# Kernel optimization log

Measured on AMD Instinct MI355X. Metric: run time of the kernel, lower is better.

The kernel has to match this reference:

```python
import jax, jax.numpy as jnp
import numpy as np
import math

BS, SEQ, EMB, BD = 4, 2048, 512, 8
H = EMB // BD


def setup_inputs() -> dict:
    key = jax.random.key(0)
    ks = jax.random.split(key, 7)
    s = lambda fan: 1.0 / np.sqrt(fan)
    x = jax.random.normal(ks[0], (BS, SEQ, EMB), jnp.float32)
    # gen_block: Linear(EMB, EMB*BD) -> ReLU -> Linear(EMB*BD, EMB*BD)
    W1 = jax.random.normal(ks[1], (EMB * BD, EMB), jnp.float32) * s(EMB)
    b1 = jnp.zeros((EMB * BD,), jnp.float32)
    W2 = jax.random.normal(ks[2], (EMB * BD, EMB * BD), jnp.float32) * s(EMB * BD)
    b2 = jnp.zeros((EMB * BD,), jnp.float32)
    # gen_value: Linear(EMB, EMB) -> ReLU -> Linear(EMB, EMB)
    V1 = jax.random.normal(ks[3], (EMB, EMB), jnp.float32) * s(EMB)
    c1 = jnp.zeros((EMB,), jnp.float32)
    V2 = jax.random.normal(ks[4], (EMB, EMB), jnp.float32) * s(EMB)
    c2 = jnp.zeros((EMB,), jnp.float32)
    a0 = jax.random.normal(ks[5], (1, H, BD), jnp.float32)
    return {"x": x, "W1": W1, "b1": b1, "W2": W2, "b2": b2,
            "V1": V1, "c1": c1, "V2": V2, "c2": c2, "a0": a0}


def _forward(x, W1, b1, W2, b2, V1, c1, V2, c2, a0):
    bs, seq_len, emb = x.shape
    bd = BD
    h = emb // bd
    # block transition matrices: [bs, seq, h, bd, bd]
    blk = jax.nn.relu(x @ W1.T + b1) @ W2.T + b2
    blk = blk.reshape(bs, seq_len, h, bd, bd)
    blk = blk - blk.mean(axis=-2, keepdims=True)
    # p=1.2 norm over rows (dim=-2), then max over columns (dim=-1)
    norm = jnp.sum(jnp.abs(blk) ** 1.2, axis=-2, keepdims=True) ** (1.0 / 1.2)
    blk = blk / jnp.max(norm, axis=-1, keepdims=True)
    # values: [bs, seq, h, bd]
    v = (jax.nn.relu(x @ V1.T + c1) @ V2.T + c2).reshape(bs, seq_len, h, bd)

    log2_L = int(math.ceil(math.log2(seq_len + 1)))
    L = 2 ** log2_L
    n_zero = L - seq_len - 1
    # prepend a0 as initial state, pad to length L
    ev = jnp.concatenate([jnp.broadcast_to(a0, (bs, h, bd))[:, None], v], axis=1)
    a = jnp.pad(ev, ((0, 0), (0, n_zero), (0, 0), (0, 0)))  # [bs, L, h, bd]
    As = jnp.pad(blk, ((0, 0), (0, n_zero), (0, 0), (0, 0), (0, 0)))[:, :, None]  # [bs, L-1, 1, h, bd, bd]

    # Blelloch-style tree scan; log2_L levels, shapes shrink along n and grow along c
    for _ in range(log2_L):
        c = As.shape[2] * 2
        a = a.reshape(bs, L // c, c, h, bd)
        a1, a2 = a[:, :, :c // 2], a[:, :, c // 2:]
        coef = As[:, ::2]          # [bs, L//c, c//2, h, bd, bd]
        remain = As[:, 1::2]       # [bs, L//c - 1, c//2, h, bd, bd]
        prodd = jnp.einsum('bnchij,bnhjk->bnchik', coef[:, 1:], remain[:, :, -1])
        remain = jnp.concatenate([remain, prodd], axis=2)
        a2 = a2 + jnp.einsum('bnchij,bnhj->bnchi', coef, a1[:, :, -1])
        a = jnp.concatenate([a1, a2], axis=2)
        As = remain

    return a.reshape(bs, L, emb)[:, 1:seq_len + 1]


def reference(x, W1, b1, W2, b2, V1, c1, V2, c2, a0):
    return _forward(x, W1, b1, W2, b2, V1, c1, V2, c2, a0)
```

## Files before the change

### kernel.cpp

```cpp
#include <hip/hip_runtime.h>
#include <hip/hip_bf16.h>
#include <cstddef>


typedef _Float16 f16;
typedef _Float16 f16x4 __attribute__((ext_vector_type(4)));
typedef _Float16 f16x8 __attribute__((ext_vector_type(8)));
typedef float f32x4 __attribute__((ext_vector_type(4)));

__global__ __launch_bounds__(256)
void split_kernel(const float* __restrict__ in, f16* __restrict__ hi,
                  f16* __restrict__ lo, int n) {
  const int idx = (blockIdx.x * 256 + threadIdx.x) * 4;
  if (idx >= n) return;
  float4 v = *(const float4*)(in + idx);
  f16x4 h, l;
  h.x = (f16)v.x; l.x = (f16)(v.x - (float)h.x);
  h.y = (f16)v.y; l.y = (f16)(v.y - (float)h.y);
  h.z = (f16)v.z; l.z = (f16)(v.z - (float)h.z);
  h.w = (f16)v.w; l.w = (f16)(v.w - (float)h.w);
  *(f16x4*)(hi + idx) = h;
  *(f16x4*)(lo + idx) = l;
}

template<int EPI>
__global__ __launch_bounds__(512, 2)
void gemm_big(const f16* __restrict__ Ahi, const f16* __restrict__ Alo,
              const f16* __restrict__ Bhi, const f16* __restrict__ Blo,
              const float* __restrict__ bias, void* __restrict__ Ov,
              int M, int N, int K, int roff) {
  __shared__ f16 S[2][4][256 * 32];
  const int tid = threadIdx.x, lane = tid & 63, wid = tid >> 6;
  const int m0 = blockIdx.y << 8, n0 = blockIdx.x << 8;
  const int wr = wid >> 2, wc = wid & 3;
  const int fr = lane & 15, g = lane >> 4;
  const int r_sub = lane >> 2, lc = lane & 3;
  const int p = wid >> 1, half = wid & 1;

  f32x4 acc[8][4];
#pragma unroll
  for (int m = 0; m < 8; ++m)
#pragma unroll
    for (int n = 0; n < 4; ++n) acc[m][n] = (f32x4)0.f;

  const f16* gsrc = (p == 0) ? Ahi + (size_t)m0 * K
                  : (p == 1) ? Alo + (size_t)m0 * K
                  : (p == 2) ? Bhi + (size_t)n0 * K
                             : Blo + (size_t)n0 * K;

  auto stage = [&](int b, int k0) {
    f16* ld = &S[b][p][half * 4096];
#pragma unroll
    for (int i = 0; i < 8; ++i) {
      const int r = half * 128 + i * 16 + r_sub;
      const int sg = (lc - r - (r >> 2)) & 3;
      const f16* sp = gsrc + (size_t)r * K + k0 + sg * 8;
      __builtin_amdgcn_global_load_lds(
          (const __attribute__((address_space(1))) unsigned int*)sp,
          (__attribute__((address_space(3))) unsigned int*)(ld + i * 512),
          16, 0, 0);
    }
  };

  const int NT = K >> 5;
  stage(0, 0);
  __syncthreads();
  int cur = 0;
  for (int t = 0; t < NT; ++t) {
    if (t + 1 < NT) stage(cur ^ 1, (t + 1) << 5);
    f16x8 ah[8], al[8], bh[4], bl[4];
#pragma unroll
    for (int m = 0; m < 8; ++m) {
      const int rr = wr * 128 + m * 16 + fr;
      const int off = rr * 32 + (((g + rr + (rr >> 2)) & 3) << 3);
      ah[m] = *(const f16x8*)&S[cur][0][off];
      al[m] = *(const f16x8*)&S[cur][1][off];
    }
#pragma unroll
    for (int n = 0; n < 4; ++n) {
      const int rr = wc * 64 + n * 16 + fr;
      const int off = rr * 32 + (((g + rr + (rr >> 2)) & 3) << 3);
      bh[n] = *(const f16x8*)&S[cur][2][off];
      bl[n] = *(const f16x8*)&S[cur][3][off];
    }
#pragma unroll
    for (int m = 0; m < 8; ++m)
#pragma unroll
      for (int n = 0; n < 4; ++n) {
        acc[m][n] = __builtin_amdgcn_mfma_f32_16x16x32_f16(ah[m], bh[n], acc[m][n], 0, 0, 0);
        acc[m][n] = __builtin_amdgcn_mfma_f32_16x16x32_f16(ah[m], bl[n], acc[m][n], 0, 0, 0);
        acc[m][n] = __builtin_amdgcn_mfma_f32_16x16x32_f16(al[m], bh[n], acc[m][n], 0, 0, 0);
      }
    __syncthreads();
    cur ^= 1;
  }

  const int fq = lane >> 4;
  float bz[4];
#pragma unroll
  for (int n = 0; n < 4; ++n) bz[n] = bias[n0 + wc * 64 + n * 16 + fr];

  if (EPI == 0) {
    f16* Ohi = (f16*)Ov;
    f16* Olo = Ohi + (size_t)M * N;
#pragma unroll
    for (int m = 0; m < 8; ++m)
#pragma unroll
      for (int n = 0; n < 4; ++n) {
        const int col = n0 + wc * 64 + n * 16 + fr;
#pragma unroll
        for (int r = 0; r < 4; ++r) {
          const int row = m0 + wr * 128 + m * 16 + fq * 4 + r;
          float v = fmaxf(acc[m][n][r] + bz[n], 0.f);
          f16 h = (f16)v;
          f16 l = (f16)(v - (float)h);
          Ohi[(size_t)row * N + col] = h;
          Olo[(size_t)row * N + col] = l;
        }
      }
  } else {
    float* O = (float*)Ov;
#pragma unroll
    for (int m = 0; m < 8; ++m) {
#pragma unroll
      for (int r = 0; r < 4; ++r) {
        float v[4];
#pragma unroll
        for (int n = 0; n < 4; ++n) v[n] = acc[m][n][r] + bz[n];
        float s = v[0] + v[1] + v[2] + v[3];
        s += __shfl_xor(s, 8);
        const float mean = s * 0.125f;
        float t = 0.f;
#pragma unroll
        for (int n = 0; n < 4; ++n) {
          v[n] -= mean;
          t += exp2f(1.2f * log2f(fabsf(v[n])));
        }
        t += __shfl_xor(t, 8);
        float nrm = exp2f((1.0f / 1.2f) * log2f(t));
        nrm = fmaxf(nrm, __shfl_xor(nrm, 1));
        nrm = fmaxf(nrm, __shfl_xor(nrm, 2));
        nrm = fmaxf(nrm, __shfl_xor(nrm, 4));
        const float inv = 1.f / nrm;
        const int row = m0 + wr * 128 + m * 16 + fq * 4 + r;
        const int grow = roff + row;
        const int bb = grow >> 11, ss = grow & 2047;
#pragma unroll
        for (int n = 0; n < 4; ++n) {
          const int col = n0 + wc * 64 + n * 16 + fr;
          O[(((size_t)(bb * 64 + (col >> 6)) * 2048 + ss) << 6) + (col & 63)] = v[n] * inv;
        }
      }
    }
  }
}

template<int EPI>
__global__ __launch_bounds__(256, 2)
void gemm_dma2(const f16* __restrict__ Ahi, const f16* __restrict__ Alo,
               const f16* __restrict__ Bhi, const f16* __restrict__ Blo,
               const float* __restrict__ bias, void* __restrict__ Ov,
               int M, int N, int K, int roff, int lg_mb) {
  __shared__ f16 S[2][4][128 * 32];
  const int tid = threadIdx.x, lane = tid & 63, wid = tid >> 6;
  const int total = gridDim.x, chunk = total >> 3;
  const int swz = (blockIdx.x & 7) * chunk + (blockIdx.x >> 3);
  const int mtile = swz & ((1 << lg_mb) - 1);
  const int ntile = swz >> lg_mb;
  const int m0 = mtile << 7, n0 = ntile << 7;
  const int wr = wid >> 1, wc = wid & 1;
  const int fr = lane & 15, g = lane >> 4;
  const int r_sub = lane >> 2, lc = lane & 3;

  f32x4 acc[4][4];
#pragma unroll
  for (int m = 0; m < 4; ++m)
#pragma unroll
    for (int n = 0; n < 4; ++n) acc[m][n] = (f32x4)0.f;

  const f16* gsrc = (wid == 0) ? Ahi + (size_t)m0 * K
                  : (wid == 1) ? Alo + (size_t)m0 * K
                  : (wid == 2) ? Bhi + (size_t)n0 * K
                               : Blo + (size_t)n0 * K;

  auto stage = [&](int b, int k0) {
    f16* ld = &S[b][wid][0];
#pragma unroll
    for (int i = 0; i < 8; ++i) {
      const int r = i * 16 + r_sub;
      const int sg = (lc - r - (r >> 2)) & 3;
      const f16* sp = gsrc + (size_t)r * K + k0 + sg * 8;
      __builtin_amdgcn_global_load_lds(
          (const __attribute__((address_space(1))) unsigned int*)sp,
          (__attribute__((address_space(3))) unsigned int*)(ld + i * 512),
          16, 0, 0);
    }
  };

  const int NT = K >> 5;
  stage(0, 0);
  __syncthreads();
  int cur = 0;
  for (int t = 0; t < NT; ++t) {
    if (t + 1 < NT) stage(cur ^ 1, (t + 1) << 5);
    f16x8 ah[4], al[4], bh[4], bl[4];
#pragma unroll
    for (int m = 0; m < 4; ++m) {
      const int rr = wr * 64 + m * 16 + fr;
      const int off = rr * 32 + (((g + rr + (rr >> 2)) & 3) << 3);
      ah[m] = *(const f16x8*)&S[cur][0][off];
      al[m] = *(const f16x8*)&S[cur][1][off];
    }
#pragma unroll
    for (int n = 0; n < 4; ++n) {
      const int rr = wc * 64 + n * 16 + fr;
      const int off = rr * 32 + (((g + rr + (rr >> 2)) & 3) << 3);
      bh[n] = *(const f16x8*)&S[cur][2][off];
      bl[n] = *(const f16x8*)&S[cur][3][off];
    }
#pragma unroll
    for (int m = 0; m < 4; ++m)
#pragma unroll
      for (int n = 0; n < 4; ++n) {
        acc[m][n] = __builtin_amdgcn_mfma_f32_16x16x32_f16(ah[m], bh[n], acc[m][n], 0, 0, 0);
        acc[m][n] = __builtin_amdgcn_mfma_f32_16x16x32_f16(ah[m], bl[n], acc[m][n], 0, 0, 0);
        acc[m][n] = __builtin_amdgcn_mfma_f32_16x16x32_f16(al[m], bh[n], acc[m][n], 0, 0, 0);
      }
    __syncthreads();
    cur ^= 1;
  }

  const int fq = lane >> 4;
  float bz[4];
#pragma unroll
  for (int n = 0; n < 4; ++n) bz[n] = bias[n0 + wc * 64 + n * 16 + fr];

  if (EPI == 0) {
    f16* Ohi = (f16*)Ov;
    f16* Olo = Ohi + (size_t)M * N;
#pragma unroll
    for (int m = 0; m < 4; ++m)
#pragma unroll
      for (int n = 0; n < 4; ++n) {
        const int col = n0 + wc * 64 + n * 16 + fr;
#pragma unroll
        for (int r = 0; r < 4; ++r) {
          const int row = m0 + wr * 64 + m * 16 + fq * 4 + r;
          float v = fmaxf(acc[m][n][r] + bz[n], 0.f);
          f16 h = (f16)v;
          f16 l = (f16)(v - (float)h);
          Ohi[(size_t)row * N + col] = h;
          Olo[(size_t)row * N + col] = l;
        }
      }
  } else {
    float* O = (float*)Ov;
#pragma unroll
    for (int m = 0; m < 4; ++m)
#pragma unroll
      for (int n = 0; n < 4; ++n) {
        const int col = n0 + wc * 64 + n * 16 + fr;
#pragma unroll
        for (int r = 0; r < 4; ++r) {
          const int row = m0 + wr * 64 + m * 16 + fq * 4 + r;
          const int grow = roff + row;
          const int bb = grow >> 11, ss = grow & 2047;
          O[(((size_t)(bb * 64 + (col >> 3)) * 2048 + ss) << 3) + (col & 7)] = acc[m][n][r] + bz[n];
        }
      }
  }
}

#define SCH2 16
#define SEGL 128
#define NSEG 16

__global__ __launch_bounds__(256)
void scan_part1(const float* __restrict__ BLKTc, const float* __restrict__ VTc,
                float* __restrict__ Msum, float* __restrict__ Csum) {
  __shared__ __align__(16) float Abuf[4][2][SCH2 * 64];
  __shared__ __align__(16) float vbuf[4][2][SCH2 * 8];
  const int w = threadIdx.x >> 6, lane = threadIdx.x & 63;
  const int id = blockIdx.x * 4 + w;
  const int stream = id >> 4, t = id & 15;
  const int i = lane >> 3, j = lane & 7;
  const float* Ab = BLKTc + (size_t)stream * (2048 * 64) + (size_t)t * (SEGL * 64);
  const float* Vb = VTc + (size_t)stream * (2048 * 8) + (size_t)t * (SEGL * 8);

  float m = (i == j) ? 1.f : 0.f;
  float cj = 0.f;

  float4 ra[4]; float2 rv;
  auto loadc = [&](int c) {
    const float* sA = Ab + c * (SCH2 * 64);
#pragma unroll
    for (int q = 0; q < 4; ++q) ra[q] = *(const float4*)(sA + q * 256 + lane * 4);
    rv = *(const float2*)(Vb + c * (SCH2 * 8) + lane * 2);
  };
  auto store_lds = [&](int slot) {
#pragma unroll
    for (int q = 0; q < 4; ++q)
      *(float4*)&Abuf[w][slot][q * 256 + lane * 4] = ra[q];
    *(float2*)&vbuf[w][slot][lane * 2] = rv;
  };

  loadc(0); store_lds(0);
  int cur = 0;
  const int NC = SEGL / SCH2;
  for (int c = 0; c < NC; ++c) {
    if (c + 1 < NC) loadc(c + 1);
#pragma unroll
    for (int s = 0; s < SCH2; ++s) {
      const float aij = Abuf[w][cur][s * 64 + lane];
      float p = aij * cj;
      p += __shfl_xor(p, 1);
      p += __shfl_xor(p, 2);
      p += __shfl_xor(p, 4);
      const float cn = p + vbuf[w][cur][s * 8 + i];
      cj = __shfl(cn, j << 3);
      float arow[8];
      *(float4*)&arow[0] = *(const float4*)&Abuf[w][cur][s * 64 + i * 8];
      *(float4*)&arow[4] = *(const float4*)&Abuf[w][cur][s * 64 + i * 8 + 4];
      float mn = 0.f;
#pragma unroll
      for (int k = 0; k < 8; ++k)
        mn = fmaf(arow[k], __shfl(m, (k << 3) | j), mn);
      m = mn;
    }
    if (c + 1 < NC) store_lds(cur ^ 1);
    cur ^= 1;
  }
  Msum[(size_t)id * 64 + lane] = m;
  if (lane < 8) Csum[(size_t)id * 8 + lane] = cj;
}

__global__ __launch_bounds__(64)
void scan_part2(const float* __restrict__ Msum, const float* __restrict__ Csum,
                const float* __restrict__ a0, float* __restrict__ Ybnd) {
  const int stream = blockIdx.x;
  const int lane = threadIdx.x;
  const int i = lane >> 3, j = lane & 7;
  const int h = stream & 63;
  float y = a0[h * 8 + j];
  for (int t = 0; t < NSEG; ++t) {
    const size_t sid = (size_t)stream * NSEG + t;
    if (lane < 8) Ybnd[sid * 8 + lane] = y;
    float p = Msum[sid * 64 + lane] * y;
    p += __shfl_xor(p, 1);
    p += __shfl_xor(p, 2);
    p += __shfl_xor(p, 4);
    const float yn = p + Csum[sid * 8 + i];
    y = __shfl(yn, j << 3);
  }
}

__global__ __launch_bounds__(256)
void scan_part3(const float* __restrict__ BLKTc, const float* __restrict__ VTc,
                const float* __restrict__ Ybnd, float* __restrict__ outc) {
  __shared__ __align__(16) float Abuf[4][2][SCH2 * 64];
  __shared__ __align__(16) float vbuf[4][2][SCH2 * 8];
  const int w = threadIdx.x >> 6, lane = threadIdx.x & 63;
  const int id = blockIdx.x * 4 + w;
  const int stream = id >> 4, t = id & 15;
  const int b = stream >> 6, h = stream & 63;
  const int i = lane >> 3, j = lane & 7;
  const float* Ab = BLKTc + (size_t)stream * (2048 * 64) + (size_t)t * (SEGL * 64);
  const float* Vb = VTc + (size_t)stream * (2048 * 8) + (size_t)t * (SEGL * 8);
  float* ob = outc + (size_t)b * (2048 * 512) + (size_t)(t * SEGL) * 512 + h * 8;

  float y = Ybnd[(size_t)id * 8 + j];

  float4 ra[4]; float2 rv;
  auto loadc = [&](int c) {
    const float* sA = Ab + c * (SCH2 * 64);
#pragma unroll
    for (int q = 0; q < 4; ++q) ra[q] = *(const float4*)(sA + q * 256 + lane * 4);
    rv = *(const float2*)(Vb + c * (SCH2 * 8) + lane * 2);
  };
  auto store_lds = [&](int slot) {
#pragma unroll
    for (int q = 0; q < 4; ++q)
      *(float4*)&Abuf[w][slot][q * 256 + lane * 4] = ra[q];
    *(float2*)&vbuf[w][slot][lane * 2] = rv;
  };

  loadc(0); store_lds(0);
  int cur = 0;
  const int NC = SEGL / SCH2;
  for (int c = 0; c < NC; ++c) {
    if (c + 1 < NC) loadc(c + 1);
#pragma unroll
    for (int s = 0; s < SCH2; ++s) {
      const float aij = Abuf[w][cur][s * 64 + lane];
      float p = aij * y;
      p += __shfl_xor(p, 1);
      p += __shfl_xor(p, 2);
      p += __shfl_xor(p, 4);
      const float yn = p + vbuf[w][cur][s * 8 + i];
      if (j == 0) ob[(size_t)(c * SCH2 + s) * 512 + i] = yn;
      y = __shfl(yn, j << 3);
    }
    if (c + 1 < NC) store_lds(cur ^ 1);
    cur ^= 1;
  }
}

extern "C" void kernel_launch(void* const* d_in, const int* in_sizes, int n_in,
                              void* d_out, int out_size, void* d_ws, size_t ws_size,
                              hipStream_t stream) {
  const float* x  = (const float*)d_in[0];
  const float* W1 = (const float*)d_in[1];
  const float* b1 = (const float*)d_in[2];
  const float* W2 = (const float*)d_in[3];
  const float* b2 = (const float*)d_in[4];
  const float* V1 = (const float*)d_in[5];
  const float* c1 = (const float*)d_in[6];
  const float* V2 = (const float*)d_in[7];
  const float* c2 = (const float*)d_in[8];
  const float* a0 = (const float*)d_in[9];
  float* out = (float*)d_out;

  dim3 blk(256);

  char* base = (char*)d_ws;
  f16* W2hi   = (f16*)base;
  f16* W2lo   = (f16*)(base + 33554432ull);
  f16* H1hi   = (f16*)(base + 67108864ull);
  float* BLKTc= (float*)(base + 134217728ull);
  float* VT   = (float*)(base + 201326592ull);
  f16* xfhi   = (f16*)(base + 218103808ull);
  f16* xflo   = (f16*)(base + 226492416ull);
  f16* W1hi   = (f16*)(base + 234881024ull);
  f16* W1lo   = (f16*)(base + 239075328ull);
  f16* V1hi   = (f16*)(base + 243269632ull);
  f16* V1lo   = (f16*)(base + 243793920ull);
  f16* V2hi   = (f16*)(base + 244318208ull);
  f16* V2lo   = (f16*)(base + 244842496ull);
  float* Msum = (float*)(base + 245366784ull);
  float* Csum = (float*)(base + 245891072ull);
  float* Ybnd = (float*)(base + 245956608ull);
  f16* HVhi   = H1hi;

  split_kernel<<<4096, blk, 0, stream>>>(x, xfhi, xflo, 4194304);
  split_kernel<<<2048, blk, 0, stream>>>(W1, W1hi, W1lo, 2097152);
  split_kernel<<<16384, blk, 0, stream>>>(W2, W2hi, W2lo, 16777216);
  split_kernel<<<256, blk, 0, stream>>>(V1, V1hi, V1lo, 262144);
  split_kernel<<<256, blk, 0, stream>>>(V2, V2hi, V2lo, 262144);

  gemm_dma2<0><<<256, blk, 0, stream>>>(
      xfhi, xflo, V1hi, V1lo, c1, HVhi, 8192, 512, 512, 0, 6);
  gemm_dma2<2><<<256, blk, 0, stream>>>(
      HVhi, HVhi + (size_t)8192 * 512, V2hi, V2lo, c2, VT, 8192, 512, 512, 0, 6);

  for (int c = 0; c < 2; ++c) {
    const f16* xahi = xfhi + (size_t)c * 4096 * 512;
    const f16* xalo = xflo + (size_t)c * 4096 * 512;
    gemm_big<0><<<dim3(16, 16), 512, 0, stream>>>(
        xahi, xalo, W1hi, W1lo, b1, H1hi, 4096, 4096, 512, 0);
    gemm_big<1><<<dim3(16, 16), 512, 0, stream>>>(
        H1hi, H1hi + (size_t)4096 * 4096, W2hi, W2lo, b2, BLKTc,
        4096, 4096, 4096, 0);
    const float* VTc = VT + (size_t)c * 2 * 64 * 2048 * 8;
    float* outc = out + (size_t)c * 2 * 2048 * 512;
    scan_part1<<<512, blk, 0, stream>>>(BLKTc, VTc, Msum, Csum);
    scan_part2<<<128, 64, 0, stream>>>(Msum, Csum, a0, Ybnd);
    scan_part3<<<512, blk, 0, stream>>>(BLKTc, VTc, Ybnd, outc);
  }
}
```

Before: 954.3 us.

## Interleave GEMM K-loop into phased LDS reads, async staging, and MFMA bursts

The GEMM main loop is split into four phases per K-tile. Each phase loads two A fragments from LDS, issues half of the next tile's global-to-LDS copies in the first two phases, and then runs an MFMA burst at raised wave priority. Explicit s_barrier, waitcnt and sched_barrier calls replace __syncthreads so memory traffic overlaps with matrix math and register pressure from fragments drops. The price is more barriers per K-tile and hand-placed wait counts that could stall or be fragile if wrong.

```diff
diff --git a/kernel.cpp b/kernel.cpp
--- a/kernel.cpp
+++ b/kernel.cpp
@@ -48,10 +48,11 @@
                   : (p == 2) ? Bhi + (size_t)n0 * K
                              : Blo + (size_t)n0 * K;
 
-  auto stage = [&](int b, int k0) {
+  auto stage_part = [&](int b, int k0, int i0) {
     f16* ld = &S[b][p][half * 4096];
 #pragma unroll
-    for (int i = 0; i < 8; ++i) {
+    for (int ii = 0; ii < 4; ++ii) {
+      const int i = i0 + ii;
       const int r = half * 128 + i * 16 + r_sub;
       const int sg = (lc - r - (r >> 2)) & 3;
       const f16* sp = gsrc + (size_t)r * K + k0 + sg * 8;
@@ -63,35 +64,56 @@
   };
 
   const int NT = K >> 5;
-  stage(0, 0);
-  __syncthreads();
+  stage_part(0, 0, 0);
+  stage_part(0, 0, 4);
+  asm volatile("s_waitcnt vmcnt(0)" ::: "memory");
+  __builtin_amdgcn_s_barrier();
+
   int cur = 0;
   for (int t = 0; t < NT; ++t) {
-    if (t + 1 < NT) stage(cur ^ 1, (t + 1) << 5);
-    f16x8 ah[8], al[8], bh[4], bl[4];
-#pragma unroll
-    for (int m = 0; m < 8; ++m) {
-      const int rr = wr * 128 + m * 16 + fr;
-      const int off = rr * 32 + (((g + rr + (rr >> 2)) & 3) << 3);
-      ah[m] = *(const f16x8*)&S[cur][0][off];
-      al[m] = *(const f16x8*)&S[cur][1][off];
-    }
-#pragma unroll
-    for (int n = 0; n < 4; ++n) {
-      const int rr = wc * 64 + n * 16 + fr;
-      const int off = rr * 32 + (((g + rr + (rr >> 2)) & 3) << 3);
-      bh[n] = *(const f16x8*)&S[cur][2][off];
-      bl[n] = *(const f16x8*)&S[cur][3][off];
-    }
-#pragma unroll
-    for (int m = 0; m < 8; ++m)
-#pragma unroll
-      for (int n = 0; n < 4; ++n) {
-        acc[m][n] = __builtin_amdgcn_mfma_f32_16x16x32_f16(ah[m], bh[n], acc[m][n], 0, 0, 0);
-        acc[m][n] = __builtin_amdgcn_mfma_f32_16x16x32_f16(ah[m], bl[n], acc[m][n], 0, 0, 0);
-        acc[m][n] = __builtin_amdgcn_mfma_f32_16x16x32_f16(al[m], bh[n], acc[m][n], 0, 0, 0);
-      }
-    __syncthreads();
+    const bool havenext = (t + 1 < NT);
+    const int nxtk0 = (t + 1) << 5;
+    f16x8 bh[4], bl[4];
+#pragma unroll
+    for (int ph = 0; ph < 4; ++ph) {
+      if (ph == 0) {
+#pragma unroll
+        for (int n = 0; n < 4; ++n) {
+          const int rr = wc * 64 + n * 16 + fr;
+          const int off = rr * 32 + (((g + rr + (rr >> 2)) & 3) << 3);
+          bh[n] = *(const f16x8*)&S[cur][2][off];
+          bl[n] = *(const f16x8*)&S[cur][3][off];
+        }
+      }
+      f16x8 ah[2], al[2];
+#pragma unroll
+      for (int mm = 0; mm < 2; ++mm) {
+        const int rr = wr * 128 + (ph * 2 + mm) * 16 + fr;
+        const int off = rr * 32 + (((g + rr + (rr >> 2)) & 3) << 3);
+        ah[mm] = *(const f16x8*)&S[cur][0][off];
+        al[mm] = *(const f16x8*)&S[cur][1][off];
+      }
+      if (havenext && ph < 2) stage_part(cur ^ 1, nxtk0, ph * 4);
+      __builtin_amdgcn_sched_barrier(0);
+      __builtin_amdgcn_s_barrier();
+      asm volatile("s_waitcnt lgkmcnt(0)" ::: "memory");
+      __builtin_amdgcn_sched_barrier(0);
+      __builtin_amdgcn_s_setprio(1);
+#pragma unroll
+      for (int mm = 0; mm < 2; ++mm)
+#pragma unroll
+        for (int n = 0; n < 4; ++n) {
+          acc[ph * 2 + mm][n] = __builtin_amdgcn_mfma_f32_16x16x32_f16(ah[mm], bh[n], acc[ph * 2 + mm][n], 0, 0, 0);
+          acc[ph * 2 + mm][n] = __builtin_amdgcn_mfma_f32_16x16x32_f16(ah[mm], bl[n], acc[ph * 2 + mm][n], 0, 0, 0);
+          acc[ph * 2 + mm][n] = __builtin_amdgcn_mfma_f32_16x16x32_f16(al[mm], bh[n], acc[ph * 2 + mm][n], 0, 0, 0);
+        }
+      __builtin_amdgcn_s_setprio(0);
+      if (ph == 3) {
+        if (havenext) asm volatile("s_waitcnt vmcnt(0)" ::: "memory");
+        __builtin_amdgcn_sched_barrier(0);
+      }
+      __builtin_amdgcn_s_barrier();
+    }
     cur ^= 1;
   }
 
```

Measured after the change: 987.9 us. 3.5% more time.
